# Performance work log

Hardware: AMD Instinct MI355X
Metric: run time of the kernel (lower is better)

The kernel has to match this reference:

```python
import jax, jax.numpy as jnp
import numpy as np

E, B, L, H1, H2, C = 8, 4096, 512, 1024, 512, 40


def setup_inputs() -> dict:
    key = jax.random.key(0)
    ks = jax.random.split(key, 9)
    return {
        "x_s": jax.random.normal(ks[0], (B, L), jnp.float32),
        "x_p": jax.random.normal(ks[1], (B, L), jnp.float32),
        "W1": jax.random.normal(ks[2], (E, 2 * L, H1), jnp.float32) / np.sqrt(2 * L).astype(np.float32),
        "b1": jax.random.normal(ks[3], (E, H1), jnp.float32) * 0.01,
        "W2": jax.random.normal(ks[4], (E, H1, H2), jnp.float32) / np.sqrt(H1).astype(np.float32),
        "b2": jax.random.normal(ks[5], (E, H2), jnp.float32) * 0.01,
        "W3": jax.random.normal(ks[6], (E, H2, C), jnp.float32) / np.sqrt(H2).astype(np.float32),
        "b3": jax.random.normal(ks[7], (E, C), jnp.float32) * 0.01,
        "sub_module_label": jax.random.randint(ks[8], (B,), 0, E, dtype=jnp.int32),
        "sub_id": 0,
    }


def reference(x_s, x_p, W1, b1, W2, b2, W3, b3, sub_module_label, sub_id):
    # Encoders (EEGNet/SCN/DCN) abstracted as identity: x_s / x_p are latent features.
    # Cls_HEAD.forward: x = cat([x_p, x_s], dim=1); per-sample routed 3-layer ELU MLP head.
    # Dropout is identity in eval mode.
    x = jnp.concatenate([x_p, x_s], axis=1)                      # [B, 2L]
    h = jax.nn.elu(jnp.einsum('bi,eih->ebh', x, W1) + b1[:, None, :])   # [E, B, H1]
    h = jax.nn.elu(jnp.einsum('ebh,ehk->ebk', h, W2) + b2[:, None, :])  # [E, B, H2]
    out_all = jnp.einsum('ebk,ekc->ebc', h, W3) + b3[:, None, :]        # [E, B, C]
    # select each sample's routed expert output
    bidx = jnp.arange(x.shape[0])
    return out_all[sub_module_label, bidx]                       # [B, C]
```

## Files before the change

### kernel.cpp

```cpp
#include <hip/hip_runtime.h>
#include <hip/hip_bf16.h>
#include <math.h>

#define En   8
#define Bn   4096
#define Ln   512
#define K1n  1024
#define H1n  1024
#define H2n  512
#define Cn   40
#define NP3  48

typedef unsigned short u16;
typedef __attribute__((ext_vector_type(8))) short bf16x8;
typedef __attribute__((ext_vector_type(4))) float f32x4;

__device__ __forceinline__ u16 f2b(float f) {
    union { float f; unsigned int u; } v; v.f = f;
    unsigned int r = v.u + 0x7FFF + ((v.u >> 16) & 1);
    return (u16)(r >> 16);
}

__device__ __forceinline__ void g2l16(const void* g, void* l) {
    __builtin_amdgcn_global_load_lds(
        (const __attribute__((address_space(1))) unsigned int*)(unsigned long long)g,
        (__attribute__((address_space(3))) unsigned int*)(unsigned int)(unsigned long long)l,
        16, 0, 0);
}

__device__ __forceinline__ void wtrans64(
    const float* __restrict__ Wsrc, u16* __restrict__ Wdst,
    int K, int N, int k0, int n0, int tid, float* sm )
{
    #pragma unroll
    for (int s = 0; s < 4; s++) {
        int idx = tid + s * 256;
        int kk = idx >> 4, c4 = (idx & 15) * 4;
        float4 v = *(const float4*)&Wsrc[(size_t)(k0 + kk) * N + n0 + c4];
        float* row = sm + kk * 65 + c4;
        row[0] = v.x; row[1] = v.y; row[2] = v.z; row[3] = v.w;
    }
    __syncthreads();
    #pragma unroll
    for (int s = 0; s < 4; s++) {
        int idx = tid + s * 256;
        int nn = idx >> 4, kc = (idx & 15) * 4;
        ushort4 o = make_ushort4(f2b(sm[(kc + 0) * 65 + nn]), f2b(sm[(kc + 1) * 65 + nn]),
                                 f2b(sm[(kc + 2) * 65 + nn]), f2b(sm[(kc + 3) * 65 + nn]));
        *(ushort4*)&Wdst[(size_t)(n0 + nn) * K + k0 + kc] = o;
    }
}

#define P1_TOT (1 + 256 + 2048)

__global__ __launch_bounds__(256) void prep1_kernel(
    const float* __restrict__ xs, const float* __restrict__ xp,
    const float* __restrict__ W1, const int* __restrict__ label,
    int* __restrict__ meta, int* __restrict__ perm,
    u16* __restrict__ Xb, u16* __restrict__ W1t)
{
    __shared__ __align__(16) float sm[64 * 65];
    const int bid = blockIdx.x;
    const int tid = threadIdx.x;

    if (bid == 0) {
        int* cnt = (int*)sm;
        int* off = cnt + En;
        if (tid < En) cnt[tid] = 0;
        __syncthreads();
        for (int b = tid; b < Bn; b += 256) atomicAdd(&cnt[label[b]], 1);
        __syncthreads();
        if (tid == 0) {
            int run = 0;
            for (int e = 0; e < En; e++) { off[e] = run; run += cnt[e]; }
            off[En] = run;
        }
        __syncthreads();
        if (tid < En) cnt[tid] = off[tid];
        __syncthreads();
        for (int b = tid; b < Bn; b += 256) {
            int e = label[b];
            perm[atomicAdd(&cnt[e], 1)] = b;
        }
        if (tid <= En) meta[tid] = off[tid];
    } else if (bid < 257) {
        int r0 = (bid - 1) * 16;
        #pragma unroll 4
        for (int s = 0; s < 16; s++) {
            int r = r0 + s;
            int k = tid * 4;
            const float* src = (k < Ln) ? (xp + (size_t)r * Ln + k)
                                        : (xs + (size_t)r * Ln + (k - Ln));
            float4 v = *(const float4*)src;
            *(ushort4*)&Xb[(size_t)r * K1n + k] =
                make_ushort4(f2b(v.x), f2b(v.y), f2b(v.z), f2b(v.w));
        }
    } else {
        int b = bid - 257;
        int e = b >> 8, rem = b & 255;
        int k0 = (rem >> 4) * 64, n0 = (rem & 15) * 64;
        wtrans64(W1 + (size_t)e * K1n * H1n, W1t + (size_t)e * H1n * K1n,
                 K1n, H1n, k0, n0, tid, sm);
    }
}

template <int K, int N, int TM, int TN, bool GATHER, bool FUSE3, bool PREP2>
__global__ __launch_bounds__(256) void mfma_gemm(
    const u16* __restrict__ A, const u16* __restrict__ Wt,
    const float* __restrict__ bias, const int* __restrict__ meta,
    const int* __restrict__ perm, u16* __restrict__ outb,
    const u16* __restrict__ Wt3, float* __restrict__ outf,
    const float* __restrict__ W2f, const float* __restrict__ W3f,
    const float* __restrict__ b3v, const int* __restrict__ labelv,
    u16* __restrict__ W2t_o, u16* __restrict__ W3t_o)
{
    constexpr int BK    = 32;
    constexpr int T     = K / BK;
    constexpr int NTC   = N / TN;
    constexpr int NTRk  = Bn / TM + En;
    constexpr int ASLOT = TM * 4;
    constexpr int BSLOT = TN * 4;
    constexpr int STAGE = ASLOT + BSLOT;
    constexpr int HSTR  = TN + 8;
    constexpr int SMST  = 2 * STAGE * 8;
    constexpr int SMU16 = (FUSE3 && (TM * HSTR) > SMST) ? (TM * HSTR) : SMST;
    __shared__ __align__(16) u16 SM[SMU16];

    const int tid = threadIdx.x;
    const int bx = blockIdx.x;

    if (PREP2 && bx >= NTRk * NTC) {
        int jb = bx - NTRk * NTC;
        if (jb < 1024) {
            int e = jb >> 7, rem = jb & 127;
            int k0 = (rem >> 3) * 64, n0 = (rem & 7) * 64;
            wtrans64(W2f + (size_t)e * H1n * H2n, W2t_o + (size_t)e * H2n * H1n,
                     H1n, H2n, k0, n0, tid, (float*)SM);
        } else if (jb < 1024 + 128) {
            int b = jb - 1024;
            int e = b >> 4, k0 = (b & 15) * 32;
            const float* src = W3f + (size_t)e * H2n * Cn;
            u16* dst = W3t_o + (size_t)e * NP3 * H2n;
            float* t = (float*)SM;
            #pragma unroll
            for (int s = 0; s < 5; s++) {
                int idx = tid + s * 256;
                int kk = idx / Cn, nn = idx - kk * Cn;
                if (kk < 32) t[kk * 41 + nn] = src[(size_t)(k0 + kk) * Cn + nn];
            }
            __syncthreads();
            #pragma unroll
            for (int s = 0; s < 6; s++) {
                int idx = tid + s * 256;
                int nn = idx >> 5, kk = idx & 31;
                float v = (nn < Cn) ? t[kk * 41 + nn] : 0.f;
                dst[(size_t)nn * H2n + k0 + kk] = f2b(v);
            }
        } else {
            int b = jb - (1024 + 128);
            int r0 = b * 64;
            #pragma unroll
            for (int s = 0; s < 10; s++) {
                int idx = tid + s * 256;
                int r = r0 + idx / Cn;
                int c = idx - (idx / Cn) * Cn;
                outf[(size_t)r * Cn + c] = b3v[labelv[r] * Cn + c];
            }
        }
        return;
    }

    const int rt = bx % NTRk;
    const int col0 = (bx / NTRk) * TN;

    int expert = -1, row0 = 0, rowmax = 0, acc_t = 0;
    int prev = meta[0];
    #pragma unroll
    for (int e = 0; e < En; e++) {
        int nxt = meta[e + 1];
        int c = nxt - prev;
        int t = (c + TM - 1) / TM;
        if (expert < 0 && rt < acc_t + t) {
            expert = e; row0 = prev + (rt - acc_t) * TM; rowmax = nxt - 1;
        }
        acc_t += t; prev = nxt;
    }
    if (expert < 0) return;

    const u16* Wexp = Wt + (size_t)expert * N * K;

    const int lane = tid & 63;
    const int wid = tid >> 6;
    const int wm = (wid & 1) * (TM / 2);
    const int wn = (wid >> 1) * (TN / 2);
    const int l15 = lane & 15;
    const int lq = lane >> 4;

    constexpr int ALOAD = ASLOT / 256;
    constexpr int BLOAD = BSLOT / 256;
    const u16* aptr[ALOAD]; int aoff[ALOAD];
    const u16* bptr[BLOAD]; int boff[BLOAD];
    #pragma unroll
    for (int s = 0; s < ALOAD; s++) {
        int idx = tid + s * 256;
        int rl = idx >> 2, c = idx & 3;
        int kq = c ^ ((rl >> 1) & 3);
        int rg = row0 + rl; if (rg > rowmax) rg = rowmax;
        if (GATHER) rg = perm[rg];
        aptr[s] = A + (size_t)rg * K + kq * 8;
        aoff[s] = idx * 8;
    }
    #pragma unroll
    for (int s = 0; s < BLOAD; s++) {
        int idx = tid + s * 256;
        int rl = idx >> 2, c = idx & 3;
        int kq = c ^ ((rl >> 1) & 3);
        bptr[s] = Wexp + (size_t)(col0 + rl) * K + kq * 8;
        boff[s] = ASLOT * 8 + idx * 8;
    }

    constexpr int MI = TM / 32;
    constexpr int NJ = TN / 32;
    f32x4 acc[MI][NJ];
    #pragma unroll
    for (int i = 0; i < MI; i++)
        #pragma unroll
        for (int j = 0; j < NJ; j++) acc[i][j] = (f32x4){0.f, 0.f, 0.f, 0.f};

    #pragma unroll
    for (int s = 0; s < ALOAD; s++) g2l16(aptr[s], &SM[aoff[s]]);
    #pragma unroll
    for (int s = 0; s < BLOAD; s++) g2l16(bptr[s], &SM[boff[s]]);

    const int cp = (lq ^ ((l15 >> 1) & 3)) * 8;

    for (int t = 0; t < T; t++) {
        __syncthreads();
        const u16* As = &SM[(t & 1) * (STAGE * 8)];
        const u16* Bs = As + ASLOT * 8;
        if (t + 1 < T) {
            int base = ((t + 1) & 1) * (STAGE * 8);
            int ko = (t + 1) * BK;
            #pragma unroll
            for (int s = 0; s < ALOAD; s++) g2l16(aptr[s] + ko, &SM[base + aoff[s]]);
            #pragma unroll
            for (int s = 0; s < BLOAD; s++) g2l16(bptr[s] + ko, &SM[base + boff[s]]);
        }
        bf16x8 af[MI], bf[NJ];
        #pragma unroll
        for (int i = 0; i < MI; i++)
            af[i] = *(const bf16x8*)&As[(wm + i * 16 + l15) * BK + cp];
        #pragma unroll
        for (int j = 0; j < NJ; j++)
            bf[j] = *(const bf16x8*)&Bs[(wn + j * 16 + l15) * BK + cp];
        #pragma unroll
        for (int i = 0; i < MI; i++)
            #pragma unroll
            for (int j = 0; j < NJ; j++)
                acc[i][j] = __builtin_amdgcn_mfma_f32_16x16x32_bf16(
                    af[i], bf[j], acc[i][j], 0, 0, 0);
    }

    if (!FUSE3) {
        #pragma unroll
        for (int i = 0; i < MI; i++) {
            #pragma unroll
            for (int j = 0; j < NJ; j++) {
                int col = col0 + wn + j * 16 + l15;
                float bv = bias[expert * N + col];
                #pragma unroll
                for (int r = 0; r < 4; r++) {
                    int grow = row0 + wm + i * 16 + lq * 4 + r;
                    if (grow <= rowmax) {
                        float v = acc[i][j][r] + bv;
                        v = (v > 0.f) ? v : (expf(v) - 1.f);
                        outb[(size_t)grow * N + col] = f2b(v);
                    }
                }
            }
        }
    } else {
        __syncthreads();
        u16* H = &SM[0];
        #pragma unroll
        for (int i = 0; i < MI; i++) {
            #pragma unroll
            for (int j = 0; j < NJ; j++) {
                int col = wn + j * 16 + l15;
                float bv = bias[expert * N + col0 + col];
                #pragma unroll
                for (int r = 0; r < 4; r++) {
                    float v = acc[i][j][r] + bv;
                    v = (v > 0.f) ? v : (expf(v) - 1.f);
                    H[(wm + i * 16 + lq * 4 + r) * HSTR + col] = f2b(v);
                }
            }
        }
        __syncthreads();
        constexpr int RI = TM / 64;
        constexpr int KC = TN / 32;
        const int rh = wid * (TM / 4);
        f32x4 a3[RI][3];
        #pragma unroll
        for (int ri = 0; ri < RI; ri++)
            #pragma unroll
            for (int j = 0; j < 3; j++) a3[ri][j] = (f32x4){0.f, 0.f, 0.f, 0.f};
        #pragma unroll
        for (int ki = 0; ki < KC; ki++) {
            bf16x8 ha[RI];
            #pragma unroll
            for (int ri = 0; ri < RI; ri++)
                ha[ri] = *(const bf16x8*)&H[(rh + ri * 16 + l15) * HSTR + ki * 32 + lq * 8];
            #pragma unroll
            for (int j = 0; j < 3; j++) {
                bf16x8 wb = *(const bf16x8*)
                    &Wt3[((size_t)expert * NP3 + j * 16 + l15) * H2n + col0 + ki * 32 + lq * 8];
                #pragma unroll
                for (int ri = 0; ri < RI; ri++)
                    a3[ri][j] = __builtin_amdgcn_mfma_f32_16x16x32_bf16(
                        ha[ri], wb, a3[ri][j], 0, 0, 0);
            }
        }
        #pragma unroll
        for (int j = 0; j < 3; j++) {
            int col = j * 16 + l15;
            if (col < Cn) {
                #pragma unroll
                for (int ri = 0; ri < RI; ri++) {
                    #pragma unroll
                    for (int r = 0; r < 4; r++) {
                        int grow = row0 + rh + ri * 16 + lq * 4 + r;
                        if (grow <= rowmax)
                            atomicAdd(&outf[(size_t)perm[grow] * Cn + col], a3[ri][j][r]);
                    }
                }
            }
        }
    }
}

extern "C" void kernel_launch(void* const* d_in, const int* in_sizes, int n_in,
                              void* d_out, int out_size, void* d_ws, size_t ws_size,
                              hipStream_t stream)
{
    const float* xs = (const float*)d_in[0];
    const float* xp = (const float*)d_in[1];
    const float* W1 = (const float*)d_in[2];
    const float* b1 = (const float*)d_in[3];
    const float* W2 = (const float*)d_in[4];
    const float* b2 = (const float*)d_in[5];
    const float* W3 = (const float*)d_in[6];
    const float* b3 = (const float*)d_in[7];
    const int* label = (const int*)d_in[8];
    float* out = (float*)d_out;

    char* ws = (char*)d_ws;
    int* meta = (int*)ws;
    int* perm = (int*)(ws + 64);
    u16* Xb  = (u16*)(ws + (64 << 10));
    u16* W1t = (u16*)(ws + (64 << 10) + (8  << 20));
    u16* W2t = (u16*)(ws + (64 << 10) + (24 << 20));
    u16* h1b = (u16*)(ws + (64 << 10) + (32 << 20));
    u16* W3t = (u16*)(ws + (64 << 10) + (40 << 20));

    prep1_kernel<<<P1_TOT, 256, 0, stream>>>(
        xs, xp, W1, label, meta, perm, Xb, W1t);

    mfma_gemm<K1n, H1n, 128, 128, true, false, true><<<320 + 1216, 256, 0, stream>>>(
        Xb, W1t, b1, meta, perm, h1b, nullptr, out,
        W2, W3, b3, label, W2t, W3t);

    mfma_gemm<H1n, H2n, 128, 64, false, true, false><<<320, 256, 0, stream>>>(
        h1b, W2t, b2, meta, perm, nullptr, W3t, out,
        nullptr, nullptr, nullptr, nullptr, nullptr, nullptr);
}
```

Measured before the change: 173.1 us.

## Triple-buffer GEMM K-loop, swizzle block order, shrink tiles for more blocks

The two-stage double-buffered K loop becomes a three-stage ring buffer. Global-to-LDS loads are issued two steps ahead, and explicit s_waitcnt vmcnt plus raw barriers let one stage stay in flight while the current one is consumed. Block indices are permuted so consecutive workgroups are spread across row tiles and column tiles. The layer-1 tile shrinks from 128x128 to 128x64 and the layer-2 tile from 128x64 to 64x64, raising block counts for better occupancy and CU fill. The cost is more LDS per block, some loss of operand reuse, and more redundant weight traffic.

Measured after the change: 171.3 us. Within noise of the previous version (-1.0%).

```diff
diff --git a/kernel.cpp b/kernel.cpp
--- a/kernel.cpp
+++ b/kernel.cpp
@@ -118,19 +118,23 @@
     constexpr int T     = K / BK;
     constexpr int NTC   = N / TN;
     constexpr int NTRk  = Bn / TM + En;
+    constexpr int NGEMM = NTRk * NTC;
     constexpr int ASLOT = TM * 4;
     constexpr int BSLOT = TN * 4;
     constexpr int STAGE = ASLOT + BSLOT;
+    constexpr int ALOAD = ASLOT / 256;
+    constexpr int BLOAD = BSLOT / 256;
+    constexpr int LW    = ALOAD + BLOAD;
     constexpr int HSTR  = TN + 8;
-    constexpr int SMST  = 2 * STAGE * 8;
+    constexpr int SMST  = 3 * STAGE * 8;
     constexpr int SMU16 = (FUSE3 && (TM * HSTR) > SMST) ? (TM * HSTR) : SMST;
     __shared__ __align__(16) u16 SM[SMU16];
 
     const int tid = threadIdx.x;
     const int bx = blockIdx.x;
 
-    if (PREP2 && bx >= NTRk * NTC) {
-        int jb = bx - NTRk * NTC;
+    if (PREP2 && bx >= NGEMM) {
+        int jb = bx - NGEMM;
         if (jb < 1024) {
             int e = jb >> 7, rem = jb & 127;
             int k0 = (rem >> 3) * 64, n0 = (rem & 7) * 64;
@@ -170,8 +174,9 @@
         return;
     }
 
-    const int rt = bx % NTRk;
-    const int col0 = (bx / NTRk) * TN;
+    const int gx = (bx & 7) * (NGEMM / 8) + (bx >> 3);
+    const int rt = gx % NTRk;
+    const int col0 = (gx / NTRk) * TN;
 
     int expert = -1, row0 = 0, rowmax = 0, acc_t = 0;
     int prev = meta[0];
@@ -196,8 +201,6 @@
     const int l15 = lane & 15;
     const int lq = lane >> 4;
 
-    constexpr int ALOAD = ASLOT / 256;
-    constexpr int BLOAD = BSLOT / 256;
     const u16* aptr[ALOAD]; int aoff[ALOAD];
     const u16* bptr[BLOAD]; int boff[BLOAD];
     #pragma unroll
@@ -227,25 +230,20 @@
         #pragma unroll
         for (int j = 0; j < NJ; j++) acc[i][j] = (f32x4){0.f, 0.f, 0.f, 0.f};
 
-    #pragma unroll
-    for (int s = 0; s < ALOAD; s++) g2l16(aptr[s], &SM[aoff[s]]);
-    #pragma unroll
-    for (int s = 0; s < BLOAD; s++) g2l16(bptr[s], &SM[boff[s]]);
-
     const int cp = (lq ^ ((l15 >> 1) & 3)) * 8;
 
-    for (int t = 0; t < T; t++) {
-        __syncthreads();
-        const u16* As = &SM[(t & 1) * (STAGE * 8)];
+    auto stage_issue = [&](int buf, int t) {
+        const int base = buf * (STAGE * 8);
+        const int ko = t * BK;
+        #pragma unroll
+        for (int s = 0; s < ALOAD; s++) g2l16(aptr[s] + ko, &SM[base + aoff[s]]);
+        #pragma unroll
+        for (int s = 0; s < BLOAD; s++) g2l16(bptr[s] + ko, &SM[base + boff[s]]);
+    };
+
+    auto kstep = [&](int buf) {
+        const u16* As = &SM[buf * (STAGE * 8)];
         const u16* Bs = As + ASLOT * 8;
-        if (t + 1 < T) {
-            int base = ((t + 1) & 1) * (STAGE * 8);
-            int ko = (t + 1) * BK;
-            #pragma unroll
-            for (int s = 0; s < ALOAD; s++) g2l16(aptr[s] + ko, &SM[base + aoff[s]]);
-            #pragma unroll
-            for (int s = 0; s < BLOAD; s++) g2l16(bptr[s] + ko, &SM[base + boff[s]]);
-        }
         bf16x8 af[MI], bf[NJ];
         #pragma unroll
         for (int i = 0; i < MI; i++)
@@ -259,7 +257,35 @@
             for (int j = 0; j < NJ; j++)
                 acc[i][j] = __builtin_amdgcn_mfma_f32_16x16x32_bf16(
                     af[i], bf[j], acc[i][j], 0, 0, 0);
-    }
+    };
+
+    stage_issue(0, 0);
+    asm volatile("" ::: "memory");
+    stage_issue(1, 1);
+    asm volatile("" ::: "memory");
+
+    int rb = 0;
+    for (int t = 0; t < T - 1; t++) {
+        if constexpr (LW == 2)
+            asm volatile("s_waitcnt vmcnt(2) lgkmcnt(0)" ::: "memory");
+        else if constexpr (LW == 3)
+            asm volatile("s_waitcnt vmcnt(3) lgkmcnt(0)" ::: "memory");
+        else
+            asm volatile("s_waitcnt vmcnt(4) lgkmcnt(0)" ::: "memory");
+        __builtin_amdgcn_s_barrier();
+        asm volatile("" ::: "memory");
+        if (t + 2 < T) {
+            int wb = rb + 2; if (wb >= 3) wb -= 3;
+            stage_issue(wb, t + 2);
+        }
+        asm volatile("" ::: "memory");
+        kstep(rb);
+        rb = (rb == 2) ? 0 : rb + 1;
+    }
+    asm volatile("s_waitcnt vmcnt(0) lgkmcnt(0)" ::: "memory");
+    __builtin_amdgcn_s_barrier();
+    asm volatile("" ::: "memory");
+    kstep(rb);
 
     if (!FUSE3) {
         #pragma unroll
@@ -366,11 +392,11 @@
     prep1_kernel<<<P1_TOT, 256, 0, stream>>>(
         xs, xp, W1, label, meta, perm, Xb, W1t);
 
-    mfma_gemm<K1n, H1n, 128, 128, true, false, true><<<320 + 1216, 256, 0, stream>>>(
+    mfma_gemm<K1n, H1n, 128, 64, true, false, true><<<640 + 1216, 256, 0, stream>>>(
         Xb, W1t, b1, meta, perm, h1b, nullptr, out,
         W2, W3, b3, label, W2t, W3t);
 
-    mfma_gemm<H1n, H2n, 128, 64, false, true, false><<<320, 256, 0, stream>>>(
+    mfma_gemm<H1n, H2n, 64, 64, false, true, false><<<576, 256, 0, stream>>>(
         h1b, W2t, b2, meta, perm, nullptr, W3t, out,
         nullptr, nullptr, nullptr, nullptr, nullptr, nullptr);
 }
```
